# Kernel optimization log

Hardware: AMD Instinct MI355X
Metric: run time of the kernel (lower is better)

Reference implementation:

```python
import jax, jax.numpy as jnp
import numpy as np

N = 131072
MUL = 32

# e3nn normalization (irrep_normalization='component', path_normalization='element'):
# alpha_path = w3j_norm * sqrt(ir_out.dim / sum_{paths into same i_out} mul1*mul2)
# 0e output: paths (0e,0e)->0e and (1o,1o)->0e -> fan = 2*32*32 = 2048
# 1o output: paths (0e,1o)->1o and (1o,0e)->1o -> fan = 2048
# 1e output: path  (1o,1o)->1e               -> fan = 1024
_A000 = 1.0 / np.sqrt(2048.0)                    # w3j(0,0,0)=1,        sqrt(1/2048)
_A011 = (1.0 / np.sqrt(3.0)) * np.sqrt(3.0 / 2048.0)   # = 1/sqrt(2048)
_A101 = _A011
_A110 = (1.0 / np.sqrt(3.0)) * np.sqrt(1.0 / 2048.0)
_A111 = (1.0 / np.sqrt(6.0)) * np.sqrt(3.0 / 1024.0)   # = 1/sqrt(2048)


def setup_inputs() -> dict:
    key = jax.random.key(0)
    ks = jax.random.split(key, 7)
    return {
        "x1": jax.random.normal(ks[0], (N, 4 * MUL), dtype=jnp.float32),
        "x2": jax.random.normal(ks[1], (N, 4 * MUL), dtype=jnp.float32),
        "w000": jax.random.normal(ks[2], (MUL, MUL, MUL), dtype=jnp.float32),
        "w011": jax.random.normal(ks[3], (MUL, MUL, MUL), dtype=jnp.float32),
        "w101": jax.random.normal(ks[4], (MUL, MUL, MUL), dtype=jnp.float32),
        "w110": jax.random.normal(ks[5], (MUL, MUL, MUL), dtype=jnp.float32),
        "w111": jax.random.normal(ks[6], (MUL, MUL, MUL), dtype=jnp.float32),
    }


def _uvw(a, b, w):
    # scalar-channel path: out_zw = sum_uv a_zu b_zv w_uvw
    return jnp.einsum('zu,zv,uvw->zw', a, b, w, optimize=True)


def _tp(x1, x2, w000, w011, w101, w110, w111):
    n = x1.shape[0]
    x1s = x1[:, :MUL]                       # [z,u]    0e
    x1v = x1[:, MUL:].reshape(n, MUL, 3)    # [z,u,3]  1o
    x2s = x2[:, :MUL]
    x2v = x2[:, MUL:].reshape(n, MUL, 3)

    # (0e,0e)->0e and (1o,1o)->0e  (w3j(1,1,0) = delta_ij/sqrt(3), folded into alpha)
    p000 = _uvw(x1s, x2s, w000)                                  # [z,w]
    p110 = jnp.einsum('zui,zvi,uvw->zw', x1v, x2v, w110, optimize=True)
    out0 = _A000 * p000 + _A110 * p110                           # [z,w]

    # (0e,1o)->1o and (1o,0e)->1o  (w3j(0,1,1) = delta/sqrt(3), folded into alpha)
    p011 = jnp.einsum('zu,zvj,uvw->zwj', x1s, x2v, w011, optimize=True)
    p101 = jnp.einsum('zui,zv,uvw->zwi', x1v, x2s, w101, optimize=True)
    out1 = _A011 * p011 + _A101 * p101                           # [z,w,3]

    # (1o,1o)->1e via levi-civita (w3j(1,1,1) = eps/sqrt(6), folded into alpha)
    # out_zwk = sum_ij eps_ijk * uvw-contraction; expand cross product per component
    comps = []
    for (i, j) in ((1, 2), (2, 0), (0, 1)):
        comps.append(_uvw(x1v[:, :, i], x2v[:, :, j], w111)
                     - _uvw(x1v[:, :, j], x2v[:, :, i], w111))
    out2 = _A111 * jnp.stack(comps, axis=-1)                     # [z,w,3]

    return jnp.concatenate(
        [out0, out1.reshape(n, -1), out2.reshape(n, -1)], axis=-1)  # [z,224]


def reference(x1, x2, w000, w011, w101, w110, w111):
    return _tp(x1, x2, w000, w011, w101, w110, w111)
```

## Files before the change

kernel.cpp:

```cpp
#include <hip/hip_runtime.h>


typedef _Float16 f16;
typedef f16 f16x8 __attribute__((ext_vector_type(8)));
typedef float f32x16 __attribute__((ext_vector_type(16)));

#define MFMA32(a, b, c) __builtin_amdgcn_mfma_f32_32x32x16_f16(a, b, c, 0, 0, 0)

#define SC_COMMON 0.022097086912079608f
#define SC_110    0.012757759118834242f

__global__ void prep_w(const float* __restrict__ w000, const float* __restrict__ w011,
                       const float* __restrict__ w101, const float* __restrict__ w110,
                       const float* __restrict__ w111, f16* __restrict__ wsW)
{
    int flat = blockIdx.x * 256 + threadIdx.x;
    if (flat >= 5 * 32768) return;
    int c    = flat >> 15;
    int r    = flat & 32767;
    int j    = r & 7;
    int lane = (r >> 3) & 63;
    int vh   = (r >> 9) & 1;
    int u    = r >> 10;
    int v = vh * 16 + ((lane >> 5) << 3) + j;
    int w = lane & 31;
    const float* src; float sc;
    switch (c) {
        case 0: src = w000; sc = SC_COMMON; break;
        case 1: src = w110; sc = SC_110;    break;
        case 2: src = w011; sc = SC_COMMON; break;
        case 3: src = w101; sc = SC_COMMON; break;
        default: src = w111; sc = SC_COMMON; break;
    }
    wsW[flat] = (f16)(sc * src[u * 1024 + v * 32 + w]);
}

template <int U0, int MODE, int NA>
__device__ __forceinline__ void do_stage(f32x16 (&acc)[NA],
                                         const f16* __restrict__ ldsW,
                                         const f16x8 (&f1g)[4][4],
                                         const f16x8 (&f2g)[4][2], int lane)
{
#pragma unroll
    for (int ul = 0; ul < 16; ++ul) {
        const int u = U0 + ul;
#pragma unroll
        for (int vh = 0; vh < 2; ++vh) {
            f16x8 b = *(const f16x8*)(ldsW + ul * 1024 + vh * 512 + lane * 8);
            if (MODE == 0) {
                f16x8 a = f1g[0][u >> 3][u & 7] * f2g[0][vh];
                acc[0] = MFMA32(a, b, acc[0]);
            } else if (MODE == 1) {
                f16x8 a = f1g[1][u >> 3][u & 7] * f2g[1][vh];
                a += f1g[2][u >> 3][u & 7] * f2g[2][vh];
                a += f1g[3][u >> 3][u & 7] * f2g[3][vh];
                acc[0] = MFMA32(a, b, acc[0]);
            } else if (MODE == 2) {
#pragma unroll
                for (int j = 0; j < 3; ++j) {
                    f16x8 a = f1g[0][u >> 3][u & 7] * f2g[1 + j][vh];
                    acc[j] = MFMA32(a, b, acc[j]);
                }
            } else if (MODE == 3) {
#pragma unroll
                for (int j = 0; j < 3; ++j) {
                    f16x8 a = f1g[1 + j][u >> 3][u & 7] * f2g[0][vh];
                    acc[j] = MFMA32(a, b, acc[j]);
                }
            } else {
#pragma unroll
                for (int k = 0; k < 3; ++k) {
                    const int P = (k == 0) ? 2 : (k == 1) ? 3 : 1;
                    const int Q = (k == 0) ? 3 : (k == 1) ? 1 : 2;
                    f16x8 a = f1g[P][u >> 3][u & 7] * f2g[Q][vh]
                            - f1g[Q][u >> 3][u & 7] * f2g[P][vh];
                    acc[k] = MFMA32(a, b, acc[k]);
                }
            }
        }
    }
}

__global__ __launch_bounds__(256, 2)
void tp_main(const float* __restrict__ x1, const float* __restrict__ x2,
             const f16* __restrict__ wsW, float* __restrict__ out)
{
    __shared__ __align__(16) f16 ldsW[2][16384];

    const int tid = threadIdx.x, lane = tid & 63, wv = tid >> 6;
    const int rowBase = blockIdx.x * 128 + wv * 32;
    const int mrow = lane & 31;
    const int half = lane >> 5;
    const int klo = half * 8;
    const float4* x1r4 = (const float4*)(x1 + (size_t)(rowBase + mrow) * 128);
    const float4* x2r4 = (const float4*)(x2 + (size_t)(rowBase + mrow) * 128);

    auto issue = [&](int buf, int s) {
        const f16* src = wsW + s * 16384;
        f16* dst = &ldsW[buf][0];
#pragma unroll
        for (int it = 0; it < 8; ++it) {
            int o = (it * 256 + tid) * 8;
            __builtin_amdgcn_global_load_lds(
                (const __attribute__((address_space(1))) void*)(src + o),
                (__attribute__((address_space(3))) void*)(dst + o), 16, 0, 0);
        }
    };

    issue(0, 0);

    f16x8 f1g[4][4];
    {
        float b0[32];
#pragma unroll
        for (int g = 0; g < 8; ++g) ((float4*)b0)[g] = x1r4[g];
#pragma unroll
        for (int g = 0; g < 4; ++g)
#pragma unroll
            for (int j = 0; j < 8; ++j) f1g[0][g][j] = (f16)b0[g * 8 + j];
        float b1[96];
#pragma unroll
        for (int g = 0; g < 24; ++g) ((float4*)b1)[g] = x1r4[8 + g];
#pragma unroll
        for (int i = 0; i < 3; ++i)
#pragma unroll
            for (int g = 0; g < 4; ++g)
#pragma unroll
                for (int j = 0; j < 8; ++j)
                    f1g[1 + i][g][j] = (f16)b1[3 * (g * 8 + j) + i];
    }

    f16x8 f2g[4][2];
    {
        float c0[16];
#pragma unroll
        for (int g = 0; g < 2; ++g) ((float4*)c0)[g]     = x2r4[klo / 4 + g];
#pragma unroll
        for (int g = 0; g < 2; ++g) ((float4*)c0)[2 + g] = x2r4[4 + klo / 4 + g];
#pragma unroll
        for (int vh = 0; vh < 2; ++vh)
#pragma unroll
            for (int j = 0; j < 8; ++j) f2g[0][vh][j] = (f16)c0[vh * 8 + j];
        float c1[48];
        const int base1 = (32 + 3 * klo) / 4;
#pragma unroll
        for (int g = 0; g < 6; ++g) ((float4*)c1)[g]     = x2r4[base1 + g];
#pragma unroll
        for (int g = 0; g < 6; ++g) ((float4*)c1)[6 + g] = x2r4[base1 + 12 + g];
#pragma unroll
        for (int i = 0; i < 3; ++i)
#pragma unroll
            for (int vh = 0; vh < 2; ++vh)
#pragma unroll
                for (int j = 0; j < 8; ++j)
                    f2g[1 + i][vh][j] = (f16)c1[vh * 24 + 3 * j + i];
    }

    __syncthreads();


    {
        f32x16 acc[1] = {};
        issue(1, 1); do_stage<0,  0>(acc, ldsW[0], f1g, f2g, lane); __syncthreads();
        issue(0, 2); do_stage<16, 0>(acc, ldsW[1], f1g, f2g, lane); __syncthreads();
        issue(1, 3); do_stage<0,  1>(acc, ldsW[0], f1g, f2g, lane); __syncthreads();
        issue(0, 4); do_stage<16, 1>(acc, ldsW[1], f1g, f2g, lane); __syncthreads();
        issue(1, 5);
#pragma unroll
        for (int reg = 0; reg < 16; ++reg) {
            int r = (reg & 3) + 8 * (reg >> 2) + 4 * half;
            out[(size_t)(rowBase + r) * 224 + mrow] = acc[0][reg];
        }
    }
    {
        f32x16 acc[3] = {};
         do_stage<0,  2>(acc, ldsW[0], f1g, f2g, lane); __syncthreads();
        issue(0, 6); do_stage<16, 2>(acc, ldsW[1], f1g, f2g, lane); __syncthreads();
        issue(1, 7); do_stage<0,  3>(acc, ldsW[0], f1g, f2g, lane); __syncthreads();
        issue(0, 8); do_stage<16, 3>(acc, ldsW[1], f1g, f2g, lane); __syncthreads();
        issue(1, 9);
#pragma unroll
        for (int reg = 0; reg < 16; ++reg) {
            int r = (reg & 3) + 8 * (reg >> 2) + 4 * half;
            size_t base = (size_t)(rowBase + r) * 224 + 32 + 3 * mrow;
            out[base + 0] = acc[0][reg];
            out[base + 1] = acc[1][reg];
            out[base + 2] = acc[2][reg];
        }
    }
    {
        f32x16 acc[3] = {};
         do_stage<0,  4>(acc, ldsW[0], f1g, f2g, lane); __syncthreads();
        do_stage<16, 4>(acc, ldsW[1], f1g, f2g, lane);
#pragma unroll
        for (int reg = 0; reg < 16; ++reg) {
            int r = (reg & 3) + 8 * (reg >> 2) + 4 * half;
            size_t base = (size_t)(rowBase + r) * 224 + 128 + 3 * mrow;
            out[base + 0] = acc[0][reg];
            out[base + 1] = acc[1][reg];
            out[base + 2] = acc[2][reg];
        }
    }
}

extern "C" void kernel_launch(void* const* d_in, const int* in_sizes, int n_in,
                              void* d_out, int out_size, void* d_ws, size_t ws_size,
                              hipStream_t stream)
{
    const float* x1   = (const float*)d_in[0];
    const float* x2   = (const float*)d_in[1];
    const float* w000 = (const float*)d_in[2];
    const float* w011 = (const float*)d_in[3];
    const float* w101 = (const float*)d_in[4];
    const float* w110 = (const float*)d_in[5];
    const float* w111 = (const float*)d_in[6];
    float* out = (float*)d_out;
    f16* wsW = (f16*)d_ws;

    hipLaunchKernelGGL(prep_w, dim3(640), dim3(256), 0, stream,
                       w000, w011, w101, w110, w111, wsW);

    int n = in_sizes[0] / 128;
    hipLaunchKernelGGL(tp_main, dim3(n / 128), dim3(256), 0, stream,
                       x1, x2, wsW, out);
}
```

Baseline: 280.2 us.

## Prefetch two weight stages ahead with explicit vmcnt waits and wave priority

Replaces __syncthreads with explicit s_waitcnt vmcnt counts and raw s_barrier so that two weight stages are in flight, letting global-to-LDS loads overlap more with MFMA work. It also raises wave priority around the MFMA stages. The hand-tuned vmcnt counts must account for the interleaved output stores; a wrong count could let a stage read LDS before its data has arrived.

```diff
diff --git a/kernel.cpp b/kernel.cpp
--- a/kernel.cpp
+++ b/kernel.cpp
@@ -81,6 +81,11 @@
     }
 }
 
+#define WAITN(N) asm volatile("s_waitcnt vmcnt(" #N ")" ::: "memory")
+#define BAR()    __builtin_amdgcn_s_barrier()
+#define PRIO1()  __builtin_amdgcn_s_setprio(1)
+#define PRIO0()  __builtin_amdgcn_s_setprio(0)
+
 __global__ __launch_bounds__(256, 2)
 void tp_main(const float* __restrict__ x1, const float* __restrict__ x2,
              const f16* __restrict__ wsW, float* __restrict__ out)
@@ -95,9 +100,9 @@
     const float4* x1r4 = (const float4*)(x1 + (size_t)(rowBase + mrow) * 128);
     const float4* x2r4 = (const float4*)(x2 + (size_t)(rowBase + mrow) * 128);
 
-    auto issue = [&](int buf, int s) {
-        const f16* src = wsW + s * 16384;
-        f16* dst = &ldsW[buf][0];
+    auto issue = [&](int s) {
+        const f16* src = wsW + (size_t)s * 16384;
+        f16* dst = &ldsW[s & 1][0];
 #pragma unroll
         for (int it = 0; it < 8; ++it) {
             int o = (it * 256 + tid) * 8;
@@ -107,7 +112,7 @@
         }
     };
 
-    issue(0, 0);
+    issue(0);
 
     f16x8 f1g[4][4];
     {
@@ -156,50 +161,62 @@
                     f2g[1 + i][vh][j] = (f16)c1[vh * 24 + 3 * j + i];
     }
 
-    __syncthreads();
-
-
-    {
-        f32x16 acc[1] = {};
-        issue(1, 1); do_stage<0,  0>(acc, ldsW[0], f1g, f2g, lane); __syncthreads();
-        issue(0, 2); do_stage<16, 0>(acc, ldsW[1], f1g, f2g, lane); __syncthreads();
-        issue(1, 3); do_stage<0,  1>(acc, ldsW[0], f1g, f2g, lane); __syncthreads();
-        issue(0, 4); do_stage<16, 1>(acc, ldsW[1], f1g, f2g, lane); __syncthreads();
-        issue(1, 5);
-#pragma unroll
-        for (int reg = 0; reg < 16; ++reg) {
-            int r = (reg & 3) + 8 * (reg >> 2) + 4 * half;
-            out[(size_t)(rowBase + r) * 224 + mrow] = acc[0][reg];
-        }
-    }
-    {
-        f32x16 acc[3] = {};
-         do_stage<0,  2>(acc, ldsW[0], f1g, f2g, lane); __syncthreads();
-        issue(0, 6); do_stage<16, 2>(acc, ldsW[1], f1g, f2g, lane); __syncthreads();
-        issue(1, 7); do_stage<0,  3>(acc, ldsW[0], f1g, f2g, lane); __syncthreads();
-        issue(0, 8); do_stage<16, 3>(acc, ldsW[1], f1g, f2g, lane); __syncthreads();
-        issue(1, 9);
-#pragma unroll
-        for (int reg = 0; reg < 16; ++reg) {
-            int r = (reg & 3) + 8 * (reg >> 2) + 4 * half;
-            size_t base = (size_t)(rowBase + r) * 224 + 32 + 3 * mrow;
-            out[base + 0] = acc[0][reg];
-            out[base + 1] = acc[1][reg];
-            out[base + 2] = acc[2][reg];
-        }
-    }
-    {
-        f32x16 acc[3] = {};
-         do_stage<0,  4>(acc, ldsW[0], f1g, f2g, lane); __syncthreads();
-        do_stage<16, 4>(acc, ldsW[1], f1g, f2g, lane);
-#pragma unroll
-        for (int reg = 0; reg < 16; ++reg) {
-            int r = (reg & 3) + 8 * (reg >> 2) + 4 * half;
-            size_t base = (size_t)(rowBase + r) * 224 + 128 + 3 * mrow;
-            out[base + 0] = acc[0][reg];
-            out[base + 1] = acc[1][reg];
-            out[base + 2] = acc[2][reg];
-        }
+    issue(1);
+
+    f32x16 acc0[1] = {};
+    f32x16 acc1[3] = {};
+    f32x16 acc2[3] = {};
+
+    WAITN(8); BAR();
+    PRIO1(); do_stage<0, 0>(acc0, ldsW[0], f1g, f2g, lane); PRIO0();
+    BAR(); issue(2);
+    WAITN(8); BAR();
+    PRIO1(); do_stage<16, 0>(acc0, ldsW[1], f1g, f2g, lane); PRIO0();
+    BAR(); issue(3);
+    WAITN(8); BAR();
+    PRIO1(); do_stage<0, 1>(acc0, ldsW[0], f1g, f2g, lane); PRIO0();
+    BAR(); issue(4);
+    WAITN(8); BAR();
+    PRIO1(); do_stage<16, 1>(acc0, ldsW[1], f1g, f2g, lane); PRIO0();
+    BAR(); issue(5);
+    WAITN(8); BAR();
+#pragma unroll
+    for (int reg = 0; reg < 16; ++reg) {
+        int r = (reg & 3) + 8 * (reg >> 2) + 4 * half;
+        out[(size_t)(rowBase + r) * 224 + mrow] = acc0[0][reg];
+    }
+    PRIO1(); do_stage<0, 2>(acc1, ldsW[0], f1g, f2g, lane); PRIO0();
+    BAR(); issue(6);
+    WAITN(24); BAR();
+    PRIO1(); do_stage<16, 2>(acc1, ldsW[1], f1g, f2g, lane); PRIO0();
+    BAR(); issue(7);
+    WAITN(8); BAR();
+    PRIO1(); do_stage<0, 3>(acc1, ldsW[0], f1g, f2g, lane); PRIO0();
+    BAR(); issue(8);
+    WAITN(8); BAR();
+    PRIO1(); do_stage<16, 3>(acc1, ldsW[1], f1g, f2g, lane); PRIO0();
+    BAR(); issue(9);
+    WAITN(8); BAR();
+#pragma unroll
+    for (int reg = 0; reg < 16; ++reg) {
+        int r = (reg & 3) + 8 * (reg >> 2) + 4 * half;
+        size_t base = (size_t)(rowBase + r) * 224 + 32 + 3 * mrow;
+        out[base + 0] = acc1[0][reg];
+        out[base + 1] = acc1[1][reg];
+        out[base + 2] = acc1[2][reg];
+    }
+    PRIO1(); do_stage<0, 4>(acc2, ldsW[0], f1g, f2g, lane); PRIO0();
+    BAR();
+    WAITN(16); BAR();
+    PRIO1(); do_stage<16, 4>(acc2, ldsW[1], f1g, f2g, lane); PRIO0();
+
+#pragma unroll
+    for (int reg = 0; reg < 16; ++reg) {
+        int r = (reg & 3) + 8 * (reg >> 2) + 4 * half;
+        size_t base = (size_t)(rowBase + r) * 224 + 128 + 3 * mrow;
+        out[base + 0] = acc2[0][reg];
+        out[base + 1] = acc2[1][reg];
+        out[base + 2] = acc2[2][reg];
     }
 }
 
```

Result: no change. 284.9 us (+1.7%).
